# Performance work log

Measured on AMD Instinct MI355X. Metric: run time of the kernel, lower is better.

The kernel has to match this reference:

```python
import jax, jax.numpy as jnp
import numpy as np

B, T, C, H = 4, 2048, 768, 12
HD = C // H
EPS = 1e-5

def _ln(x, s, b):
    m = jnp.mean(x, axis=-1, keepdims=True)
    v = jnp.mean(jnp.square(x - m), axis=-1, keepdims=True)
    return (x - m) * jax.lax.rsqrt(v + EPS) * s + b

def setup_inputs() -> dict:
    key = jax.random.key(0)
    ks = jax.random.split(key, 8)
    x = jax.random.normal(ks[0], (B, T, C), dtype=jnp.float32)
    mask = jnp.tril(jnp.ones((T, T), dtype=bool))[None, None, :, :]  # causal [1,1,T,T]
    s = lambda fan_in: 1.0 / np.sqrt(fan_in)
    return {
        "x": x,
        "mask": mask,
        "ln1_s": jnp.ones((C,), jnp.float32),
        "ln1_b": jnp.zeros((C,), jnp.float32),
        "w_attn": jax.random.normal(ks[1], (C, 3 * C), jnp.float32) * s(C),
        "b_attn": jnp.zeros((3 * C,), jnp.float32),
        "w_o": jax.random.normal(ks[2], (C, C), jnp.float32) * s(C),
        "b_o": jnp.zeros((C,), jnp.float32),
        "ln2_s": jnp.ones((C,), jnp.float32),
        "ln2_b": jnp.zeros((C,), jnp.float32),
        "w_fc": jax.random.normal(ks[3], (C, 4 * C), jnp.float32) * s(C),
        "b_fc": jnp.zeros((4 * C,), jnp.float32),
        "w_proj": jax.random.normal(ks[4], (4 * C, C), jnp.float32) * s(4 * C),
        "b_proj": jnp.zeros((C,), jnp.float32),
    }

def reference(x, mask, ln1_s, ln1_b, w_attn, b_attn, w_o, b_o,
              ln2_s, ln2_b, w_fc, b_fc, w_proj, b_proj):
    # --- attention branch (pre-LN) ---
    h = _ln(x, ln1_s, ln1_b)
    qkv = (h @ w_attn + b_attn).reshape(B, T, 3 * H, HD)
    q, k, v = jnp.array_split(qkv, 3, axis=2)  # each [B,T,H,HD]
    scale = 1.0 / jnp.sqrt(jnp.float32(HD))
    attn = jnp.einsum('bqhd,bkhd->bhqk', q, k) * scale
    attn = jnp.where(mask, attn, jnp.finfo(jnp.float32).min)
    attn = jax.nn.softmax(attn, axis=-1)
    ctx = jnp.einsum('bhqk,bkhd->bqhd', attn, v).reshape(B, T, C)
    x = x + ctx @ w_o + b_o
    # --- MLP branch (pre-LN) ---
    h = _ln(x, ln2_s, ln2_b)
    h = jax.nn.gelu(h @ w_fc + b_fc, approximate=True)
    x = x + h @ w_proj + b_proj
    return x
```

## Files before the change

### kernel.cpp

```cpp
#include <hip/hip_runtime.h>


typedef unsigned short u16;
typedef unsigned int u32;
typedef __attribute__((ext_vector_type(8))) short short8;
typedef __attribute__((ext_vector_type(4))) float f32x4;
typedef __attribute__((ext_vector_type(16))) float f32x16;

__device__ __forceinline__ u16 f2bf(float f) {
    union { float f; unsigned u; } v; v.f = f;
    unsigned u = v.u;
    unsigned r = (u + 0x7FFFu + ((u >> 16) & 1u)) >> 16;
    return (u16)r;
}

__device__ __forceinline__ u32 cvtpk_bf16(float lo, float hi) {
    u32 r;
    asm("v_cvt_pk_bf16_f32 %0, %1, %2" : "=v"(r) : "v"(lo), "v"(hi));
    return r;
}

__device__ __forceinline__ void gld16(const u16* g, u16* l) {
    __builtin_amdgcn_global_load_lds(
        (const __attribute__((address_space(1))) void*)g,
        (__attribute__((address_space(3))) void*)l, 16, 0, 0);
}

__global__ void transpose_bf16_kernel(const float* __restrict__ w,
                                      u16* __restrict__ wt, int K, int N) {
    __shared__ float t[32][33];
    int n0 = blockIdx.x * 32, k0 = blockIdx.y * 32;
    int tx = threadIdx.x, ty = threadIdx.y;
#pragma unroll
    for (int i = 0; i < 4; i++)
        t[ty + 8 * i][tx] = w[(size_t)(k0 + ty + 8 * i) * N + n0 + tx];
    __syncthreads();
#pragma unroll
    for (int i = 0; i < 4; i++)
        wt[(size_t)(n0 + ty + 8 * i) * K + k0 + tx] = f2bf(t[tx][ty + 8 * i]);
}

__global__ void ln_kernel(const float* __restrict__ x, const float* __restrict__ s,
                          const float* __restrict__ b, u16* __restrict__ out) {
    int row = blockIdx.x;
    int tid = threadIdx.x;
    const float* xr = x + (size_t)row * 768;
    float v0 = xr[tid], v1 = xr[tid + 256], v2 = xr[tid + 512];
    float sum = v0 + v1 + v2;
    float sq = v0 * v0 + v1 * v1 + v2 * v2;
#pragma unroll
    for (int off = 32; off; off >>= 1) {
        sum += __shfl_down(sum, off);
        sq += __shfl_down(sq, off);
    }
    __shared__ float red[8];
    int wid = tid >> 6, lane = tid & 63;
    if (lane == 0) { red[wid] = sum; red[4 + wid] = sq; }
    __syncthreads();
    if (tid == 0) {
        float s4 = red[0] + red[1] + red[2] + red[3];
        float q4 = red[4] + red[5] + red[6] + red[7];
        red[0] = s4 * (1.0f / 768.0f);
        red[1] = q4 * (1.0f / 768.0f);
    }
    __syncthreads();
    float mean = red[0];
    float var = red[1] - mean * mean;
    float rstd = rsqrtf(var + 1e-5f);
    u16* orow = out + (size_t)row * 768;
    orow[tid]       = f2bf((v0 - mean) * rstd * s[tid]       + b[tid]);
    orow[tid + 256] = f2bf((v1 - mean) * rstd * s[tid + 256] + b[tid + 256]);
    orow[tid + 512] = f2bf((v2 - mean) * rstd * s[tid + 512] + b[tid + 512]);
}

template <int GELU, int RES, int OUTMODE>
__global__ __launch_bounds__(256) void gemm_kernel(
    const u16* __restrict__ A, const u16* __restrict__ Wt,
    const float* __restrict__ bias, const float* __restrict__ res,
    void* __restrict__ out, int M, int N, int K,
    u16* __restrict__ qbuf, u16* __restrict__ kbuf, u16* __restrict__ vbuf) {
    __shared__ __align__(16) u16 lA[128 * 64];
    __shared__ __align__(16) u16 lB[128 * 64];
    int m0 = blockIdx.x * 128, n0 = blockIdx.y * 128;
    int tid = threadIdx.x;
    int wid = tid >> 6, lane = tid & 63;
    int wr = wid >> 1, wc = wid & 1;
    int l15 = lane & 15, lhi = lane >> 4;

    const u16* aptr[4];
    const u16* bptr[4];
#pragma unroll
    for (int s = 0; s < 4; s++) {
        int u = s * 256 + tid;
        int row = u >> 3;
        int c8 = (u & 7) ^ (row & 7);
        aptr[s] = A + (size_t)(m0 + row) * K + c8 * 8;
        bptr[s] = Wt + (size_t)(n0 + row) * K + c8 * 8;
    }

    f32x4 acc[4][4];
#pragma unroll
    for (int i = 0; i < 4; i++)
#pragma unroll
        for (int j = 0; j < 4; j++) acc[i][j] = (f32x4)0.0f;

    for (int k0 = 0; k0 < K; k0 += 64) {
#pragma unroll
        for (int s = 0; s < 4; s++) gld16(aptr[s] + k0, &lA[(s * 256 + tid) * 8]);
#pragma unroll
        for (int s = 0; s < 4; s++) gld16(bptr[s] + k0, &lB[(s * 256 + tid) * 8]);
        __syncthreads();
        short8 af[2][4], bfr[2][4];
#pragma unroll
        for (int ks = 0; ks < 2; ks++)
#pragma unroll
            for (int f = 0; f < 4; f++) {
                int ra = wr * 64 + f * 16 + l15;
                af[ks][f] = *(const short8*)&lA[ra * 64 + (((ks * 4 + lhi) ^ (ra & 7)) << 3)];
                int rb = wc * 64 + f * 16 + l15;
                bfr[ks][f] = *(const short8*)&lB[rb * 64 + (((ks * 4 + lhi) ^ (rb & 7)) << 3)];
            }
#pragma unroll
        for (int ks = 0; ks < 2; ks++)
#pragma unroll
            for (int fm = 0; fm < 4; fm++)
#pragma unroll
                for (int fn = 0; fn < 4; fn++)
                    acc[fm][fn] = __builtin_amdgcn_mfma_f32_16x16x32_bf16(
                        af[ks][fm], bfr[ks][fn], acc[fm][fn], 0, 0, 0);
        __syncthreads();
    }
    if (OUTMODE == 2) {
        int region = n0 / 768;
#pragma unroll
        for (int fm = 0; fm < 4; fm++)
#pragma unroll
            for (int fn = 0; fn < 4; fn++) {
                int col = n0 + wc * 64 + fn * 16 + l15;
                float bv = bias[col];
                int c = col - region * 768;
                int h = c >> 6, d = c & 63;
#pragma unroll
                for (int r = 0; r < 4; r++) {
                    int row = m0 + wr * 64 + fm * 16 + lhi * 4 + r;
                    int bb = row >> 11, t = row & 2047;
                    u16 val = f2bf(acc[fm][fn][r] + bv);
                    size_t bh = (size_t)bb * 12 + h;
                    if (region == 0)      qbuf[(bh * 2048 + t) * 64 + d] = val;
                    else if (region == 1) kbuf[(bh * 2048 + t) * 64 + d] = val;
                    else                  vbuf[(bh * 64 + d) * 2048 + t] = val;
                }
            }
    } else {
#pragma unroll
        for (int fm = 0; fm < 4; fm++)
#pragma unroll
            for (int fn = 0; fn < 4; fn++) {
                int col = n0 + wc * 64 + fn * 16 + l15;
                float bv = bias[col];
#pragma unroll
                for (int r = 0; r < 4; r++) {
                    int row = m0 + wr * 64 + fm * 16 + lhi * 4 + r;
                    float v = acc[fm][fn][r] + bv;
                    if (RES) v += res[(size_t)row * N + col];
                    if (GELU) {
                        float z = 0.7978845608028654f * (v + 0.044715f * v * v * v);
                        v = 0.5f * v * (1.0f + tanhf(z));
                    }
                    if (OUTMODE == 1)
                        ((u16*)out)[(size_t)row * N + col] = f2bf(v);
                    else
                        ((float*)out)[(size_t)row * N + col] = v;
                }
            }
    }
}

__global__ __launch_bounds__(256) void attn_kernel(const u16* __restrict__ qbuf,
                                                   const u16* __restrict__ kbuf,
                                                   const u16* __restrict__ vbuf,
                                                   u16* __restrict__ ctx) {
    int bid = blockIdx.x;
    int qt = 15 - (bid / 48);
    int bh = bid % 48;
    int b = bh / 12, h = bh % 12;
    int q0 = qt * 128;
    int tid = threadIdx.x, wid = tid >> 6, lane = tid & 63;
    int l31 = lane & 31, hi = lane >> 5;

    __shared__ __align__(16) u16 lK[64 * 64];
    __shared__ __align__(16) u16 lV[64 * 64];

    const size_t bhT = (size_t)bh * 2048;

    const u16* kp[2];
    const u16* vp[2];
#pragma unroll
    for (int s = 0; s < 2; s++) {
        int u = s * 256 + tid;
        int row = u >> 3;
        int c8 = (u & 7) ^ (row & 7);
        kp[s] = kbuf + (bhT + row) * 64 + c8 * 8;
        vp[s] = vbuf + ((size_t)bh * 64 + row) * 2048 + c8 * 8;
    }

    int qrow = q0 + wid * 32 + l31;
    short8 bq[4];
#pragma unroll
    for (int ks = 0; ks < 4; ks++)
        bq[ks] = *(const short8*)(qbuf + (bhT + qrow) * 64 + ks * 16 + hi * 8);

    f32x16 oacc[2];
#pragma unroll
    for (int dt = 0; dt < 2; dt++) oacc[dt] = (f32x16)0.0f;
    float mb = -1e30f, lr = 0.0f;
    const float C2 = 0.125f * 1.44269504089f;
    const float THR = 11.55f;
    int myq = q0 + wid * 32 + l31;
    int qmax = q0 + wid * 32 + 31;

    int nt = 2 * qt + 2;
    for (int t = 0; t < nt; t++) {
        int k0 = t * 64;
#pragma unroll
        for (int s = 0; s < 2; s++) gld16(kp[s] + (size_t)k0 * 64, &lK[(s * 256 + tid) * 8]);
#pragma unroll
        for (int s = 0; s < 2; s++) gld16(vp[s] + k0, &lV[(s * 256 + tid) * 8]);
        __syncthreads();

        if (k0 <= qmax) {
            f32x16 sa[2];
#pragma unroll
            for (int kt = 0; kt < 2; kt++) sa[kt] = (f32x16)0.0f;
#pragma unroll
            for (int kt = 0; kt < 2; kt++) {
                int rk = kt * 32 + l31;
#pragma unroll
                for (int ks = 0; ks < 4; ks++) {
                    short8 ak = *(const short8*)&lK[rk * 64 + (((ks * 2 + hi) ^ (rk & 7)) << 3)];
                    sa[kt] = __builtin_amdgcn_mfma_f32_32x32x16_bf16(ak, bq[ks], sa[kt], 0, 0, 0);
                }
            }
            if (k0 + 63 > q0 + wid * 32) {
#pragma unroll
                for (int kt = 0; kt < 2; kt++)
#pragma unroll
                    for (int r = 0; r < 16; r++) {
                        int key = k0 + kt * 32 + (r & 3) + 8 * (r >> 2) + 4 * hi;
                        if (key > myq) sa[kt][r] = -1e30f;
                    }
            }
            float tmax = -1e30f;
#pragma unroll
            for (int kt = 0; kt < 2; kt++)
#pragma unroll
                for (int r = 0; r < 16; r++) tmax = fmaxf(tmax, sa[kt][r]);
            tmax = fmaxf(tmax, __shfl_xor(tmax, 32));
            float tmb = tmax * C2;
            if (__any(tmb > mb + THR)) {
                float mbn = fmaxf(mb, tmb);
                float corr = __builtin_amdgcn_exp2f(mb - mbn);
#pragma unroll
                for (int r = 0; r < 16; r++) {
                    int qm = (r & 3) + 8 * (r >> 2) + 4 * hi;
                    float c = __shfl(corr, qm);
                    oacc[0][r] *= c;
                    oacc[1][r] *= c;
                }
                lr *= corr;
                mb = mbn;
            }
            float rs = 0.0f;
#pragma unroll
            for (int kt = 0; kt < 2; kt++)
#pragma unroll
                for (int r = 0; r < 16; r++) {
                    float pv = __builtin_amdgcn_exp2f(fmaf(sa[kt][r], C2, -mb));
                    sa[kt][r] = pv;
                    rs += pv;
                }
            rs += __shfl_xor(rs, 32);
            lr += rs;
            short8 pa[4];
#pragma unroll
            for (int kt = 0; kt < 2; kt++)
#pragma unroll
                for (int ks2 = 0; ks2 < 2; ks2++) {
                    int base = ks2 * 8;
                    u32 A0 = cvtpk_bf16(sa[kt][base + 0], sa[kt][base + 1]);
                    u32 B0 = cvtpk_bf16(sa[kt][base + 4], sa[kt][base + 5]);
                    u32 A1 = cvtpk_bf16(sa[kt][base + 2], sa[kt][base + 3]);
                    u32 B1 = cvtpk_bf16(sa[kt][base + 6], sa[kt][base + 7]);
                    u32 A0s = (u32)__shfl_xor((int)A0, 32);
                    u32 B0s = (u32)__shfl_xor((int)B0, 32);
                    u32 A1s = (u32)__shfl_xor((int)A1, 32);
                    u32 B1s = (u32)__shfl_xor((int)B1, 32);
                    union { u32 u[4]; short8 s; } w;
                    w.u[0] = hi ? B0s : A0;
                    w.u[1] = hi ? B1s : A1;
                    w.u[2] = hi ? B0 : A0s;
                    w.u[3] = hi ? B1 : A1s;
                    pa[kt * 2 + ks2] = w.s;
                }
#pragma unroll
            for (int kt = 0; kt < 2; kt++)
#pragma unroll
                for (int ks2 = 0; ks2 < 2; ks2++) {
                    short8 ap = pa[kt * 2 + ks2];
#pragma unroll
                    for (int dt = 0; dt < 2; dt++) {
                        int rd = dt * 32 + l31;
                        short8 bv = *(const short8*)&lV[rd * 64 + (((kt * 4 + ks2 * 2 + hi) ^ (rd & 7)) << 3)];
                        oacc[dt] = __builtin_amdgcn_mfma_f32_32x32x16_bf16(ap, bv, oacc[dt], 0, 0, 0);
                    }
                }
        }
        __syncthreads();
    }
    const size_t rowb = (size_t)b * 2048;
    float inv = 1.0f / lr;
#pragma unroll
    for (int r = 0; r < 16; r++) {
        int qm = (r & 3) + 8 * (r >> 2) + 4 * hi;
        float ir = __shfl(inv, qm);
        int row = q0 + wid * 32 + qm;
        u16* op = ctx + (rowb + row) * 768 + h * 64 + l31;
        op[0]  = f2bf(oacc[0][r] * ir);
        op[32] = f2bf(oacc[1][r] * ir);
    }
}

extern "C" void kernel_launch(void* const* d_in, const int* in_sizes, int n_in,
                              void* d_out, int out_size, void* d_ws, size_t ws_size,
                              hipStream_t stream) {
    const float* x      = (const float*)d_in[0];
    const float* ln1_s  = (const float*)d_in[2];
    const float* ln1_b  = (const float*)d_in[3];
    const float* w_attn = (const float*)d_in[4];
    const float* b_attn = (const float*)d_in[5];
    const float* w_o    = (const float*)d_in[6];
    const float* b_o    = (const float*)d_in[7];
    const float* ln2_s  = (const float*)d_in[8];
    const float* ln2_b  = (const float*)d_in[9];
    const float* w_fc   = (const float*)d_in[10];
    const float* b_fc   = (const float*)d_in[11];
    const float* w_proj = (const float*)d_in[12];
    const float* b_proj = (const float*)d_in[13];

    char* ws = (char*)d_ws;
    u16* wT_attn = (u16*)(ws + 0);
    u16* wT_o    = (u16*)(ws + 3538944);
    u16* wT_fc   = (u16*)(ws + 4718592);
    u16* wT_proj = (u16*)(ws + 9437184);
    u16* bufA    = (u16*)(ws + 14155776);
    u16* qbuf    = (u16*)(ws + 26738688);
    u16* kbuf    = (u16*)(ws + 39321600);
    u16* vbuf    = (u16*)(ws + 51904512);
    u16* act     = (u16*)(ws + 26738688);
    float* x1    = (float*)(ws + 77070336);

    dim3 tb(32, 8);
    transpose_bf16_kernel<<<dim3(2304 / 32, 768 / 32), tb, 0, stream>>>(w_attn, wT_attn, 768, 2304);
    transpose_bf16_kernel<<<dim3(768 / 32, 768 / 32), tb, 0, stream>>>(w_o, wT_o, 768, 768);
    transpose_bf16_kernel<<<dim3(3072 / 32, 768 / 32), tb, 0, stream>>>(w_fc, wT_fc, 768, 3072);
    transpose_bf16_kernel<<<dim3(768 / 32, 3072 / 32), tb, 0, stream>>>(w_proj, wT_proj, 3072, 768);

    ln_kernel<<<8192, 256, 0, stream>>>(x, ln1_s, ln1_b, bufA);
    gemm_kernel<0, 0, 2><<<dim3(64, 18), 256, 0, stream>>>(bufA, wT_attn, b_attn, nullptr, nullptr,
                                                           8192, 2304, 768, qbuf, kbuf, vbuf);
    attn_kernel<<<768, 256, 0, stream>>>(qbuf, kbuf, vbuf, bufA);
    gemm_kernel<0, 1, 0><<<dim3(64, 6), 256, 0, stream>>>(bufA, wT_o, b_o, x, x1,
                                                          8192, 768, 768, nullptr, nullptr, nullptr);
    ln_kernel<<<8192, 256, 0, stream>>>(x1, ln2_s, ln2_b, bufA);
    gemm_kernel<1, 0, 1><<<dim3(64, 24), 256, 0, stream>>>(bufA, wT_fc, b_fc, nullptr, act,
                                                           8192, 3072, 768, nullptr, nullptr, nullptr);
    gemm_kernel<0, 1, 0><<<dim3(64, 6), 256, 0, stream>>>(act, wT_proj, b_proj, x1, (float*)d_out,
                                                          8192, 768, 3072, nullptr, nullptr, nullptr);
}
```

Before: 292.1 us.

## Double-buffer LDS tiles in GEMM and attention; use exp2-based GELU

Both the GEMM and the attention kernels now keep two LDS buffers per operand. The next K (or key/value) tile is fetched with global_load_lds before the MFMA work on the current tile, so global-to-LDS latency overlaps compute, and one barrier per iteration remains instead of two. The tanh GELU is rewritten in its equivalent sigmoid form using hardware exp2 and reciprocal intrinsics, avoiding the costly tanhf. Doubling shared memory (64 KB per GEMM block) may lower occupancy, and the fast intrinsics are slightly less accurate.

```diff
diff --git a/kernel.cpp b/kernel.cpp
--- a/kernel.cpp
+++ b/kernel.cpp
@@ -24,6 +24,13 @@
     __builtin_amdgcn_global_load_lds(
         (const __attribute__((address_space(1))) void*)g,
         (__attribute__((address_space(3))) void*)l, 16, 0, 0);
+}
+
+__device__ __forceinline__ float gelu_fast(float v) {
+    float t = v * v;
+    float z2n = v * (-2.3022078f - 0.10294376f * t);
+    float e = __builtin_amdgcn_exp2f(z2n);
+    return v * __builtin_amdgcn_rcpf(1.0f + e);
 }
 
 __global__ void transpose_bf16_kernel(const float* __restrict__ w,
@@ -79,8 +86,8 @@
     const float* __restrict__ bias, const float* __restrict__ res,
     void* __restrict__ out, int M, int N, int K,
     u16* __restrict__ qbuf, u16* __restrict__ kbuf, u16* __restrict__ vbuf) {
-    __shared__ __align__(16) u16 lA[128 * 64];
-    __shared__ __align__(16) u16 lB[128 * 64];
+    __shared__ __align__(16) u16 lA[2][128 * 64];
+    __shared__ __align__(16) u16 lB[2][128 * 64];
     int m0 = blockIdx.x * 128, n0 = blockIdx.y * 128;
     int tid = threadIdx.x;
     int wid = tid >> 6, lane = tid & 63;
@@ -104,21 +111,31 @@
 #pragma unroll
         for (int j = 0; j < 4; j++) acc[i][j] = (f32x4)0.0f;
 
-    for (int k0 = 0; k0 < K; k0 += 64) {
-#pragma unroll
-        for (int s = 0; s < 4; s++) gld16(aptr[s] + k0, &lA[(s * 256 + tid) * 8]);
-#pragma unroll
-        for (int s = 0; s < 4; s++) gld16(bptr[s] + k0, &lB[(s * 256 + tid) * 8]);
-        __syncthreads();
+#pragma unroll
+    for (int s = 0; s < 4; s++) gld16(aptr[s], &lA[0][(s * 256 + tid) * 8]);
+#pragma unroll
+    for (int s = 0; s < 4; s++) gld16(bptr[s], &lB[0][(s * 256 + tid) * 8]);
+    __syncthreads();
+
+    int KT = K >> 6;
+    int cur = 0;
+    for (int t = 0; t < KT; t++) {
+        if (t + 1 < KT) {
+            int ko = (t + 1) << 6;
+#pragma unroll
+            for (int s = 0; s < 4; s++) gld16(aptr[s] + ko, &lA[cur ^ 1][(s * 256 + tid) * 8]);
+#pragma unroll
+            for (int s = 0; s < 4; s++) gld16(bptr[s] + ko, &lB[cur ^ 1][(s * 256 + tid) * 8]);
+        }
         short8 af[2][4], bfr[2][4];
 #pragma unroll
         for (int ks = 0; ks < 2; ks++)
 #pragma unroll
             for (int f = 0; f < 4; f++) {
                 int ra = wr * 64 + f * 16 + l15;
-                af[ks][f] = *(const short8*)&lA[ra * 64 + (((ks * 4 + lhi) ^ (ra & 7)) << 3)];
+                af[ks][f] = *(const short8*)&lA[cur][ra * 64 + (((ks * 4 + lhi) ^ (ra & 7)) << 3)];
                 int rb = wc * 64 + f * 16 + l15;
-                bfr[ks][f] = *(const short8*)&lB[rb * 64 + (((ks * 4 + lhi) ^ (rb & 7)) << 3)];
+                bfr[ks][f] = *(const short8*)&lB[cur][rb * 64 + (((ks * 4 + lhi) ^ (rb & 7)) << 3)];
             }
 #pragma unroll
         for (int ks = 0; ks < 2; ks++)
@@ -129,7 +146,9 @@
                     acc[fm][fn] = __builtin_amdgcn_mfma_f32_16x16x32_bf16(
                         af[ks][fm], bfr[ks][fn], acc[fm][fn], 0, 0, 0);
         __syncthreads();
-    }
+        cur ^= 1;
+    }
+
     if (OUTMODE == 2) {
         int region = n0 / 768;
 #pragma unroll
@@ -163,10 +182,7 @@
                     int row = m0 + wr * 64 + fm * 16 + lhi * 4 + r;
                     float v = acc[fm][fn][r] + bv;
                     if (RES) v += res[(size_t)row * N + col];
-                    if (GELU) {
-                        float z = 0.7978845608028654f * (v + 0.044715f * v * v * v);
-                        v = 0.5f * v * (1.0f + tanhf(z));
-                    }
+                    if (GELU) v = gelu_fast(v);
                     if (OUTMODE == 1)
                         ((u16*)out)[(size_t)row * N + col] = f2bf(v);
                     else
@@ -188,8 +204,8 @@
     int tid = threadIdx.x, wid = tid >> 6, lane = tid & 63;
     int l31 = lane & 31, hi = lane >> 5;
 
-    __shared__ __align__(16) u16 lK[64 * 64];
-    __shared__ __align__(16) u16 lV[64 * 64];
+    __shared__ __align__(16) u16 lK[2][64 * 64];
+    __shared__ __align__(16) u16 lV[2][64 * 64];
 
     const size_t bhT = (size_t)bh * 2048;
 
@@ -220,14 +236,22 @@
     int qmax = q0 + wid * 32 + 31;
 
     int nt = 2 * qt + 2;
+#pragma unroll
+    for (int s = 0; s < 2; s++) gld16(kp[s], &lK[0][(s * 256 + tid) * 8]);
+#pragma unroll
+    for (int s = 0; s < 2; s++) gld16(vp[s], &lV[0][(s * 256 + tid) * 8]);
+    __syncthreads();
+
+    int cur = 0;
     for (int t = 0; t < nt; t++) {
         int k0 = t * 64;
-#pragma unroll
-        for (int s = 0; s < 2; s++) gld16(kp[s] + (size_t)k0 * 64, &lK[(s * 256 + tid) * 8]);
-#pragma unroll
-        for (int s = 0; s < 2; s++) gld16(vp[s] + k0, &lV[(s * 256 + tid) * 8]);
-        __syncthreads();
-
+        if (t + 1 < nt) {
+            int kn = (t + 1) * 64;
+#pragma unroll
+            for (int s = 0; s < 2; s++) gld16(kp[s] + (size_t)kn * 64, &lK[cur ^ 1][(s * 256 + tid) * 8]);
+#pragma unroll
+            for (int s = 0; s < 2; s++) gld16(vp[s] + kn, &lV[cur ^ 1][(s * 256 + tid) * 8]);
+        }
         if (k0 <= qmax) {
             f32x16 sa[2];
 #pragma unroll
@@ -237,7 +261,7 @@
                 int rk = kt * 32 + l31;
 #pragma unroll
                 for (int ks = 0; ks < 4; ks++) {
-                    short8 ak = *(const short8*)&lK[rk * 64 + (((ks * 2 + hi) ^ (rk & 7)) << 3)];
+                    short8 ak = *(const short8*)&lK[cur][rk * 64 + (((ks * 2 + hi) ^ (rk & 7)) << 3)];
                     sa[kt] = __builtin_amdgcn_mfma_f32_32x32x16_bf16(ak, bq[ks], sa[kt], 0, 0, 0);
                 }
             }
@@ -310,12 +334,13 @@
 #pragma unroll
                     for (int dt = 0; dt < 2; dt++) {
                         int rd = dt * 32 + l31;
-                        short8 bv = *(const short8*)&lV[rd * 64 + (((kt * 4 + ks2 * 2 + hi) ^ (rd & 7)) << 3)];
+                        short8 bv = *(const short8*)&lV[cur][rd * 64 + (((kt * 4 + ks2 * 2 + hi) ^ (rd & 7)) << 3)];
                         oacc[dt] = __builtin_amdgcn_mfma_f32_32x32x16_bf16(ap, bv, oacc[dt], 0, 0, 0);
                     }
                 }
         }
         __syncthreads();
+        cur ^= 1;
     }
     const size_t rowb = (size_t)b * 2048;
     float inv = 1.0f / lr;
```

Measured after the change: 263.0 us. 10.0% less time.
